# Kernel tuning notes

Measured on AMD Instinct MI355X. Metric: run time of the kernel, lower is better.

Reference implementation:

```python
import jax, jax.numpy as jnp
import numpy as np

N = 4096      # nodes
FEAT = 512    # feature_size
HID = 256     # hidden_dim
E = 131072    # edges (avg degree 32)


def setup_inputs() -> dict:
    key = jax.random.key(0)
    ks = jax.random.split(key, 10)
    x = jax.random.normal(ks[0], (N, FEAT), dtype=jnp.float32)
    edge_index = jax.random.randint(ks[1], (2, E), 0, N)
    edge_attr = jax.random.uniform(ks[2], (E, 1), dtype=jnp.float32)
    # nn.Linear(bias=False) weights, stored as [in, out] so k = x @ Wk
    Wk = jax.random.normal(ks[3], (FEAT, HID), dtype=jnp.float32) / np.sqrt(FEAT)
    Wq = jax.random.normal(ks[4], (FEAT, HID), dtype=jnp.float32) / np.sqrt(FEAT)
    Wv = jax.random.normal(ks[5], (FEAT, FEAT), dtype=jnp.float32) / np.sqrt(FEAT)
    # EmbeddingTable.reset_parameters: normal(0, 1), shape [num_embeddings=2, dim]
    Ek = jax.random.normal(ks[6], (2, HID), dtype=jnp.float32)
    Eq = jax.random.normal(ks[7], (2, HID), dtype=jnp.float32)
    Ev = jax.random.normal(ks[8], (2, FEAT), dtype=jnp.float32)
    # ContinuousEmbeddingIndex params
    idx_bias = jnp.full((1,), 0.5, dtype=jnp.float32)
    idx_mult = jnp.full((1,), 10.0, dtype=jnp.float32)
    return dict(x=x, edge_index=edge_index, edge_attr=edge_attr,
                Wk=Wk, Wq=Wq, Wv=Wv, Ek=Ek, Eq=Eq, Ev=Ev,
                idx_bias=idx_bias, idx_mult=idx_mult)


def reference(x, edge_index, edge_attr, Wk, Wq, Wv, Ek, Eq, Ev, idx_bias, idx_mult):
    n = x.shape[0]
    L = x.shape[-1]  # feature_size, used as softmax scale
    src, dst = edge_index[0], edge_index[1]

    # ContinuousEmbeddingIndex: soft 2-way interpolation weights [E, 2]
    s = jax.nn.sigmoid((edge_attr - idx_bias) * idx_mult)
    w = jnp.concatenate([s, 1.0 - s], axis=-1)

    # per-edge relative embeddings (EmbeddingTable: weights @ embeddings)
    rk = w @ Ek   # [E, HID]
    rq = w @ Eq   # [E, HID]
    rv = w @ Ev   # [E, FEAT]

    k = x @ Wk    # [N, HID]
    q = x @ Wq    # [N, HID]
    v = x @ Wv    # [N, FEAT]

    # A = q k^T + (q_i . Rk_ij) + (k_j . Rq_ij) + q k^T
    # The Rk/Rq terms are nonzero only on edges -> compute per-edge and scatter-add
    # (to_dense_adj sums duplicate edges, matched by .add).
    A = 2.0 * (q @ k.T)                                   # [N, N]
    edge_bias = jnp.sum(q[src] * rk, axis=-1) + jnp.sum(k[dst] * rq, axis=-1)  # [E]
    A = A.at[src, dst].add(edge_bias)
    A = jax.nn.softmax(A / np.sqrt(L), axis=-1)           # dropout = identity (eval)

    # M = A v + sum_j A_ij * Rv_ij  (second term only nonzero on edges)
    M = A @ v
    M = M + jax.ops.segment_sum(A[src, dst][:, None] * rv, src, num_segments=n)
    return M
```

## Files before the change

kernel.cpp:

```cpp
#include <hip/hip_runtime.h>
#include <hip/hip_bf16.h>
#include <cmath>


typedef short bf16x8 __attribute__((ext_vector_type(8)));
typedef float f32x4  __attribute__((ext_vector_type(4)));
typedef unsigned short ushort_t;
typedef unsigned short ushort8v __attribute__((ext_vector_type(8)));

constexpr int BUCKET = 64;

__device__ __forceinline__ ushort_t f2bf(float f) {
    union { float f; unsigned u; } v; v.f = f;
    unsigned u = v.u;
    u += 0x7FFFu + ((u >> 16) & 1u);
    return (ushort_t)(u >> 16);
}
__device__ __forceinline__ float bf2f(ushort_t h) {
    union { unsigned u; float f; } v; v.u = ((unsigned)h) << 16;
    return v.f;
}
__device__ __forceinline__ ushort_t f2h(float f) {
    union { _Float16 h; ushort_t u; } v; v.h = (_Float16)f; return v.u;
}
__device__ __forceinline__ float h2f(ushort_t u) {
    union { ushort_t u; _Float16 h; } v; v.u = u; return (float)v.h;
}
__device__ __forceinline__ void gload_lds16(const void* g, void* l) {
    __builtin_amdgcn_global_load_lds(
        (const __attribute__((address_space(1))) void*)g,
        (__attribute__((address_space(3))) void*)l, 16, 0, 0);
}

__device__ __forceinline__ void gemm_core(
    const ushort_t* __restrict__ A, const ushort_t* __restrict__ B,
    int lda, int ldb, int Ksz, size_t kbase, int bm, int bn,
    ushort_t* As, ushort_t* Bs, f32x4 (&acc)[4][4])
{
    constexpr int BK = 32;
    const int tid  = threadIdx.x;
    const int lane = tid & 63;
    const int wid  = tid >> 6;
    const int wm = (wid >> 1) * 64;
    const int wn = (wid & 1) * 64;

    const int r0 = tid >> 2;
    const int c8 = (tid & 3) * 8;
    const ushort_t* Ag0 = A + (size_t)(bm + r0) * lda + kbase + c8;
    const ushort_t* Bg0 = B + (size_t)(bn + r0) * ldb + kbase + c8;
    const ushort_t* Ag1 = Ag0 + (size_t)64 * lda;
    const ushort_t* Bg1 = Bg0 + (size_t)64 * ldb;
    ushort_t* AsW0 = &As[(wid * 64) * 8];
    ushort_t* AsW1 = &As[(256 + wid * 64) * 8];
    ushort_t* BsW0 = &Bs[(wid * 64) * 8];
    ushort_t* BsW1 = &Bs[(256 + wid * 64) * 8];

    const int fr = lane & 15;
    const int kh = (lane >> 4) * 8;

    for (int k0 = 0; k0 < Ksz; k0 += BK) {
        gload_lds16(Ag0 + k0, AsW0);
        gload_lds16(Ag1 + k0, AsW1);
        gload_lds16(Bg0 + k0, BsW0);
        gload_lds16(Bg1 + k0, BsW1);
        __syncthreads();

        bf16x8 af[4], bfv[4];
        #pragma unroll
        for (int i = 0; i < 4; ++i) {
            af[i]  = *(const bf16x8*)&As[(wm + i * 16 + fr) * 32 + kh];
            bfv[i] = *(const bf16x8*)&Bs[(wn + i * 16 + fr) * 32 + kh];
        }
        #pragma unroll
        for (int i = 0; i < 4; ++i)
            #pragma unroll
            for (int j = 0; j < 4; ++j)
                acc[i][j] = __builtin_amdgcn_mfma_f32_16x16x32_bf16(
                    af[i], bfv[j], acc[i][j], 0, 0, 0);
        __syncthreads();
    }
}

__device__ __forceinline__ int swizzle_bid()
{
    int bid = blockIdx.y * gridDim.x + blockIdx.x;
    const int nwg = gridDim.x * gridDim.y;
    if ((nwg & 7) == 0) {
        const int cpx = nwg >> 3;
        bid = (bid & 7) * cpx + (bid >> 3);
    }
    return bid;
}

template<int MODE>
__global__ __launch_bounds__(256) void gemm_nt_mfma(
    const ushort_t* __restrict__ A, const ushort_t* __restrict__ B,
    void* __restrict__ Cv, int lda, int ldb, int ldc, int Ksz, float alpha)
{
    __shared__ ushort_t As[128 * 32];
    __shared__ ushort_t Bs[128 * 32];
    const int bid = swizzle_bid();
    const int bm = (bid / gridDim.x) * 128;
    const int bn = (bid % gridDim.x) * 128;
    f32x4 acc[4][4] = {};
    gemm_core(A, B, lda, ldb, Ksz, 0, bm, bn, As, Bs, acc);

    const int lane = threadIdx.x & 63;
    const int wid  = threadIdx.x >> 6;
    const int wm = (wid >> 1) * 64, wn = (wid & 1) * 64;
    const int cr = (lane >> 4) * 4, cc = lane & 15;
    #pragma unroll
    for (int i = 0; i < 4; ++i)
        #pragma unroll
        for (int j = 0; j < 4; ++j) {
            const int col = bn + wn + j * 16 + cc;
            const int rowb = bm + wm + i * 16 + cr;
            #pragma unroll
            for (int jj = 0; jj < 4; ++jj) {
                const float val = alpha * acc[i][j][jj];
                if (MODE == 0)
                    ((float*)Cv)[(size_t)(rowb + jj) * ldc + col] = val;
                else if (MODE == 1)
                    ((ushort_t*)Cv)[(size_t)(rowb + jj) * ldc + col] = f2bf(val);
                else
                    ((ushort_t*)Cv)[(size_t)(rowb + jj) * ldc + col] = f2h(val);
            }
        }
}

__global__ __launch_bounds__(256) void proj_gemm(
    const ushort_t* __restrict__ xb, const ushort_t* __restrict__ Wqkt,
    const ushort_t* __restrict__ Wvt, ushort_t* __restrict__ qkb,
    ushort_t* __restrict__ vTb, int FEAT, int HID, int N)
{
    __shared__ ushort_t As[128 * 32];
    __shared__ ushort_t Bs[128 * 32];
    const int b = blockIdx.x;
    const ushort_t* A; const ushort_t* B; ushort_t* C;
    int bm, bn, ldc;
    if (b < 128) {
        const int gx = (2 * HID) / 128;
        bm = (b / gx) * 128; bn = (b % gx) * 128;
        A = xb; B = Wqkt; C = qkb; ldc = 2 * HID;
    } else {
        const int b2 = b - 128;
        const int gx = N / 128;
        bm = (b2 / gx) * 128; bn = (b2 % gx) * 128;
        A = Wvt; B = xb; C = vTb; ldc = N;
    }
    f32x4 acc[4][4] = {};
    gemm_core(A, B, FEAT, FEAT, FEAT, 0, bm, bn, As, Bs, acc);

    const int lane = threadIdx.x & 63;
    const int wid  = threadIdx.x >> 6;
    const int wm = (wid >> 1) * 64, wn = (wid & 1) * 64;
    const int cr = (lane >> 4) * 4, cc = lane & 15;
    #pragma unroll
    for (int i = 0; i < 4; ++i)
        #pragma unroll
        for (int j = 0; j < 4; ++j) {
            const int col = bn + wn + j * 16 + cc;
            const int rowb = bm + wm + i * 16 + cr;
            #pragma unroll
            for (int jj = 0; jj < 4; ++jj)
                C[(size_t)(rowb + jj) * ldc + col] = f2bf(acc[i][j][jj]);
        }
}

__global__ __launch_bounds__(256) void pv_gemm_splitk(
    const ushort_t* __restrict__ P, const ushort_t* __restrict__ vT,
    ushort_t* __restrict__ parts, int N, int FEAT, int Kchunk)
{
    __shared__ ushort_t As[128 * 32];
    __shared__ ushort_t Bs[128 * 32];
    const int bid = swizzle_bid();
    const int bm = (bid / gridDim.x) * 128;
    const int bn = (bid % gridDim.x) * 128;

    f32x4 acc[4][4] = {};
    gemm_core(P, vT, N, N, Kchunk, (size_t)blockIdx.z * Kchunk, bm, bn, As, Bs, acc);

    const int tid = threadIdx.x;
    const int lane = tid & 63;
    const int wid  = tid >> 6;
    const int wm = (wid >> 1) * 64, wn = (wid & 1) * 64;
    const int cr = (lane >> 4) * 4, cc = lane & 15;
    ushort_t* myPart = parts + (size_t)blockIdx.z * N * FEAT;
    #pragma unroll
    for (int i = 0; i < 4; ++i)
        #pragma unroll
        for (int j = 0; j < 4; ++j) {
            const int col = bn + wn + j * 16 + cc;
            const int rowb = bm + wm + i * 16 + cr;
            #pragma unroll
            for (int jj = 0; jj < 4; ++jj)
                myPart[(size_t)(rowb + jj) * FEAT + col] = f2bf(acc[i][j][jj]);
        }
}

__global__ void reduce_add_rv_kernel(
    const ushort_t* __restrict__ parts, float* __restrict__ out,
    const float* __restrict__ c0, const float* __restrict__ c1,
    const float* __restrict__ Ev, int FEAT, size_t zstride, int nz)
{
    const int i8 = blockIdx.x * 256 + threadIdx.x;
    const int F8 = FEAT / 8;
    const int node = i8 / F8;
    const int f0 = (i8 % F8) * 8;
    float s[8] = {};
    for (int z = 0; z < nz; ++z) {
        const ushort8v p = *(const ushort8v*)(parts + (size_t)z * zstride + (size_t)i8 * 8);
        #pragma unroll
        for (int j = 0; j < 8; ++j) s[j] += bf2f(p[j]);
    }
    const float a0 = c0[node], a1 = c1[node];
    float4 o0, o1;
    const float4 e00 = *(const float4*)(Ev + f0);
    const float4 e01 = *(const float4*)(Ev + f0 + 4);
    const float4 e10 = *(const float4*)(Ev + FEAT + f0);
    const float4 e11 = *(const float4*)(Ev + FEAT + f0 + 4);
    o0.x = s[0] + a0 * e00.x + a1 * e10.x;
    o0.y = s[1] + a0 * e00.y + a1 * e10.y;
    o0.z = s[2] + a0 * e00.z + a1 * e10.z;
    o0.w = s[3] + a0 * e00.w + a1 * e10.w;
    o1.x = s[4] + a0 * e01.x + a1 * e11.x;
    o1.y = s[5] + a0 * e01.y + a1 * e11.y;
    o1.z = s[6] + a0 * e01.z + a1 * e11.z;
    o1.w = s[7] + a0 * e01.w + a1 * e11.w;
    float* op = out + (size_t)node * FEAT + f0;
    *(float4*)op = o0;
    *(float4*)(op + 4) = o1;
}

__global__ __launch_bounds__(256) void prep_kernel(
    const float* __restrict__ x, const float* __restrict__ Wq,
    const float* __restrict__ Wk, const float* __restrict__ Wv,
    ushort_t* __restrict__ xb, ushort_t* __restrict__ Wqkt,
    ushort_t* __restrict__ Wvt, int* __restrict__ rowcnt,
    int N, int FEAT, int HID)
{
    const int b = blockIdx.x;
    const int tid = threadIdx.x;
    const int xBlocks = (N * FEAT / 8) / 256;
    const int qkTiles = (FEAT / 32) * (HID / 32);
    const int vTiles  = (FEAT / 32) * (FEAT / 32);
    const int zBase = xBlocks + 2 * qkTiles + vTiles;

    if (b >= zBase) {
        const int i = (b - zBase) * 256 + tid;
        if (i <= N) rowcnt[i] = 0;
        return;
    }
    if (b < xBlocks) {
        const int i = b * 256 + tid;
        const float4 a = ((const float4*)x)[2 * i];
        const float4 c = ((const float4*)x)[2 * i + 1];
        ushort8v o;
        o[0] = f2bf(a.x); o[1] = f2bf(a.y); o[2] = f2bf(a.z); o[3] = f2bf(a.w);
        o[4] = f2bf(c.x); o[5] = f2bf(c.y); o[6] = f2bf(c.z); o[7] = f2bf(c.w);
        ((ushort8v*)xb)[i] = o;
        return;
    }

    __shared__ float tile[32][33];
    int t = b - xBlocks;
    const float* src; ushort_t* dst; int I, O;
    if (t < qkTiles)            { src = Wq; dst = Wqkt;                       I = FEAT; O = HID; }
    else if (t < 2 * qkTiles)   { src = Wk; dst = Wqkt + (size_t)HID * FEAT;  I = FEAT; O = HID; t -= qkTiles; }
    else                        { src = Wv; dst = Wvt;                        I = FEAT; O = FEAT; t -= 2 * qkTiles; }
    const int ot = O / 32;
    const int r0 = (t / ot) * 32;
    const int c0 = (t % ot) * 32;
    const int lr = tid >> 5;
    const int lc = tid & 31;
    #pragma unroll
    for (int rr = 0; rr < 32; rr += 8)
        tile[lr + rr][lc] = src[(size_t)(r0 + lr + rr) * O + c0 + lc];
    __syncthreads();
    #pragma unroll
    for (int rr = 0; rr < 32; rr += 8)
        dst[(size_t)(c0 + lr + rr) * I + r0 + lc] = f2bf(tile[lc][lr + rr]);
}

__global__ __launch_bounds__(256) void node_dots(
    const ushort_t* __restrict__ qk,
    const float* __restrict__ Ek, const float* __restrict__ Eq,
    float* qk0, float* qk1, float* kq0, float* kq1, int HID)
{
    const int node = blockIdx.x;
    const int t = threadIdx.x;
    const ushort_t* row = qk + (size_t)node * (2 * HID);
    const float qv = bf2f(row[t]);
    const float kv = bf2f(row[HID + t]);
    float p0 = qv * Ek[t];
    float p1 = qv * Ek[HID + t];
    float p2 = kv * Eq[t];
    float p3 = kv * Eq[HID + t];
    #pragma unroll
    for (int off = 32; off > 0; off >>= 1) {
        p0 += __shfl_down(p0, off);
        p1 += __shfl_down(p1, off);
        p2 += __shfl_down(p2, off);
        p3 += __shfl_down(p3, off);
    }
    __shared__ float red[4][4];
    if ((t & 63) == 0) {
        const int w = t >> 6;
        red[w][0] = p0; red[w][1] = p1; red[w][2] = p2; red[w][3] = p3;
    }
    __syncthreads();
    if (t == 0) {
        qk0[node] = red[0][0] + red[1][0] + red[2][0] + red[3][0];
        qk1[node] = red[0][1] + red[1][1] + red[2][1] + red[3][1];
        kq0[node] = red[0][2] + red[1][2] + red[2][2] + red[3][2];
        kq1[node] = red[0][3] + red[1][3] + red[2][3] + red[3][3];
    }
}

__global__ void scatter_kernel(
    const int* __restrict__ ei, const float* __restrict__ attr,
    const float* __restrict__ qk0, const float* __restrict__ qk1,
    const float* __restrict__ kq0, const float* __restrict__ kq1,
    int* __restrict__ rowcnt, int4* __restrict__ ebuf, int4* __restrict__ oflow,
    int E, int N, float scale,
    const float* __restrict__ ibp, const float* __restrict__ imp)
{
    const int e = blockIdx.x * 256 + threadIdx.x;
    if (e >= E) return;
    const int src = ei[e];
    const int dst = ei[E + e];
    const float s = 1.f / (1.f + __expf(-(attr[e] - ibp[0]) * imp[0]));
    const float bias = (s * qk0[src] + (1.f - s) * qk1[src]
                      + s * kq0[dst] + (1.f - s) * kq1[dst]) * scale;
    const int pos = atomicAdd(&rowcnt[src], 1);
    if (pos < BUCKET) {
        int4 rec; rec.x = dst; rec.y = __float_as_int(bias);
        rec.z = __float_as_int(s); rec.w = 0;
        ebuf[(size_t)src * BUCKET + pos] = rec;
    } else {
        const int oi = atomicAdd(&rowcnt[N], 1);
        int4 rec; rec.x = src; rec.y = dst;
        rec.z = __float_as_int(bias); rec.w = __float_as_int(s);
        oflow[oi] = rec;
    }
}

__global__ __launch_bounds__(256) void softmax_rows_bf16(
    const ushort_t* __restrict__ Ah, const int* __restrict__ rowcnt,
    const int4* __restrict__ ebuf, const int4* __restrict__ oflow,
    ushort_t* __restrict__ P, float* __restrict__ c0, float* __restrict__ c1,
    int N)
{
    __shared__ float lbias[4096];
    __shared__ float red[4];
    __shared__ float csum[2];
    const int r = blockIdx.x;
    const ushort_t* a = Ah + (size_t)r * N;
    ushort_t* p = P + (size_t)r * N;
    const int t = threadIdx.x;

    #pragma unroll
    for (int u = 0; u < 4; ++u)
        *(float4*)&lbias[(u * 256 + t) * 4] = float4{0.f, 0.f, 0.f, 0.f};
    if (t < 2) csum[t] = 0.f;

    float v[16];
    {
        const ushort8v h0 = ((const ushort8v*)a)[t];
        const ushort8v h1 = ((const ushort8v*)a)[256 + t];
        #pragma unroll
        for (int j = 0; j < 8; ++j) { v[j] = h2f(h0[j]); v[8 + j] = h2f(h1[j]); }
    }
    __syncthreads();

    const int cnt = min(rowcnt[r], BUCKET);
    if (t < cnt) {
        const int4 rec = ebuf[(size_t)r * BUCKET + t];
        atomicAdd(&lbias[rec.x], __int_as_float(rec.y));
    }
    const int ocnt = rowcnt[N];
    for (int j = t; j < ocnt; j += 256) {
        const int4 rec = oflow[j];
        if (rec.x == r) atomicAdd(&lbias[rec.y], __int_as_float(rec.z));
    }
    __syncthreads();

    float mx = -1e30f;
    {
        const int b0 = t * 8, b1 = (256 + t) * 8;
        const float4 l0 = *(const float4*)&lbias[b0];
        const float4 l1 = *(const float4*)&lbias[b0 + 4];
        const float4 l2 = *(const float4*)&lbias[b1];
        const float4 l3 = *(const float4*)&lbias[b1 + 4];
        v[0] += l0.x; v[1] += l0.y; v[2]  += l0.z; v[3]  += l0.w;
        v[4] += l1.x; v[5] += l1.y; v[6]  += l1.z; v[7]  += l1.w;
        v[8] += l2.x; v[9] += l2.y; v[10] += l2.z; v[11] += l2.w;
        v[12] += l3.x; v[13] += l3.y; v[14] += l3.z; v[15] += l3.w;
    }
    #pragma unroll
    for (int j = 0; j < 16; ++j) mx = fmaxf(mx, v[j]);
    #pragma unroll
    for (int off = 32; off > 0; off >>= 1) mx = fmaxf(mx, __shfl_down(mx, off));
    if ((t & 63) == 0) red[t >> 6] = mx;
    __syncthreads();
    const float m = fmaxf(fmaxf(red[0], red[1]), fmaxf(red[2], red[3]));
    __syncthreads();

    float sum = 0.f;
    #pragma unroll
    for (int j = 0; j < 16; ++j) { v[j] = __expf(v[j] - m); sum += v[j]; }
    #pragma unroll
    for (int off = 32; off > 0; off >>= 1) sum += __shfl_down(sum, off);
    if ((t & 63) == 0) red[t >> 6] = sum;
    __syncthreads();
    const float inv = 1.f / (red[0] + red[1] + red[2] + red[3]);

    ushort8v o0, o1;
    {
        const int b0 = t * 8, b1 = (256 + t) * 8;
        #pragma unroll
        for (int j = 0; j < 8; ++j) {
            const float p0 = v[j] * inv;
            const float p1 = v[8 + j] * inv;
            o0[j] = f2bf(p0);
            o1[j] = f2bf(p1);
            lbias[b0 + j] = p0;
            lbias[b1 + j] = p1;
        }
    }
    ((ushort8v*)p)[t] = o0;
    ((ushort8v*)p)[256 + t] = o1;
    __syncthreads();

    if (t < cnt) {
        const int4 rec = ebuf[(size_t)r * BUCKET + t];
        const float s = __int_as_float(rec.z);
        const float pv = lbias[rec.x];
        atomicAdd(&csum[0], pv * s);
        atomicAdd(&csum[1], pv * (1.f - s));
    }
    for (int j = t; j < ocnt; j += 256) {
        const int4 rec = oflow[j];
        if (rec.x == r) {
            const float s = __int_as_float(rec.w);
            const float pv = lbias[rec.y];
            atomicAdd(&csum[0], pv * s);
            atomicAdd(&csum[1], pv * (1.f - s));
        }
    }
    __syncthreads();
    if (t == 0) { c0[r] = csum[0]; c1[r] = csum[1]; }
}

extern "C" void kernel_launch(void* const* d_in, const int* in_sizes, int n_in,
                              void* d_out, int out_size, void* d_ws, size_t ws_size,
                              hipStream_t stream)
{
    const float* x    = (const float*)d_in[0];
    const int*   ei   = (const int*)d_in[1];
    const float* attr = (const float*)d_in[2];
    const float* Wk   = (const float*)d_in[3];
    const float* Wq   = (const float*)d_in[4];
    const float* Wv   = (const float*)d_in[5];
    const float* Ek   = (const float*)d_in[6];
    const float* Eq   = (const float*)d_in[7];
    const float* Ev   = (const float*)d_in[8];
    const float* ib   = (const float*)d_in[9];
    const float* im   = (const float*)d_in[10];
    float* out = (float*)d_out;

    const int FEAT = (int)lroundf(sqrtf((float)in_sizes[5]));
    const int HID  = in_sizes[3] / FEAT;
    const int N    = in_sizes[0] / FEAT;
    const int E    = in_sizes[2];

    char* w = (char*)d_ws;
    size_t o = 0;
    ushort_t* xb   = (ushort_t*)(w + o); o += (size_t)N * FEAT * 2;
    ushort_t* Wqkt = (ushort_t*)(w + o); o += (size_t)2 * HID * FEAT * 2;
    ushort_t* Wvt  = (ushort_t*)(w + o); o += (size_t)FEAT * FEAT * 2;
    ushort_t* qkb  = (ushort_t*)(w + o); o += (size_t)N * 2 * HID * 2;
    ushort_t* vTb  = (ushort_t*)(w + o); o += (size_t)FEAT * N * 2;
    ushort_t* Ah   = (ushort_t*)(w + o); o += (size_t)N * N * 2;
    ushort_t* Pb   = (ushort_t*)(w + o); o += (size_t)N * N * 2;
    float*    qk0  = (float*)(w + o);    o += (size_t)N * 4;
    float*    qk1  = (float*)(w + o);    o += (size_t)N * 4;
    float*    kq0  = (float*)(w + o);    o += (size_t)N * 4;
    float*    kq1  = (float*)(w + o);    o += (size_t)N * 4;
    float*    c0   = (float*)(w + o);    o += (size_t)N * 4;
    float*    c1   = (float*)(w + o);    o += (size_t)N * 4;
    int*      rowcnt = (int*)(w + o);    o += (size_t)(N + 8) * 4;
    o = (o + 15) & ~(size_t)15;
    int4*     ebuf   = (int4*)(w + o);   o += (size_t)N * BUCKET * 16;
    int4*     oflow  = (int4*)(w + o);   o += (size_t)E * 16;
    ushort_t* pvpart = Ah;

    const dim3 blk(256);
    const int NZ = 4;
    const int Kchunk = N / NZ;
    const float scale = 1.f / sqrtf((float)FEAT);

    const int xBlocks = (N * FEAT / 8) / 256;
    const int qkTiles = (FEAT / 32) * (HID / 32);
    const int vTiles  = (FEAT / 32) * (FEAT / 32);
    const int zBlocks = (N + 1 + 255) / 256;
    prep_kernel<<<xBlocks + 2 * qkTiles + vTiles + zBlocks, blk, 0, stream>>>(
        x, Wq, Wk, Wv, xb, Wqkt, Wvt, rowcnt, N, FEAT, HID);

    proj_gemm<<<256, blk, 0, stream>>>(xb, Wqkt, Wvt, qkb, vTb, FEAT, HID, N);

    node_dots<<<N, blk, 0, stream>>>(qkb, Ek, Eq, qk0, qk1, kq0, kq1, HID);

    scatter_kernel<<<(E + 255) / 256, blk, 0, stream>>>(
        ei, attr, qk0, qk1, kq0, kq1, rowcnt, ebuf, oflow, E, N, scale, ib, im);

    gemm_nt_mfma<2><<<dim3(N / 128, N / 128), blk, 0, stream>>>(
        qkb, qkb + HID, Ah, 2 * HID, 2 * HID, N, HID, 2.f * scale);

    softmax_rows_bf16<<<N, blk, 0, stream>>>(Ah, rowcnt, ebuf, oflow, Pb, c0, c1, N);

    pv_gemm_splitk<<<dim3(FEAT / 128, N / 128, NZ), blk, 0, stream>>>(
        Pb, vTb, pvpart, N, FEAT, Kchunk);

    reduce_add_rv_kernel<<<(N * FEAT / 8) / 256, blk, 0, stream>>>(
        pvpart, out, c0, c1, Ev, FEAT, (size_t)N * FEAT, NZ);
}
```

Before: 118.5 us.

## Fuse node dot products into projection GEMM and merge scatter with QK GEMM

Computes the per-node Ek/Eq dot products in the projection GEMM epilogue, using 16-lane shuffle reductions followed by atomicAdd into zeroed buffers, and drops the separate node_dots kernel. The edge scatter and the QK^T GEMM are merged into one launch, with extra blocks beyond the GEMM tiles doing the scatter. This removes two kernel launches and lets the scatter's small blocks run alongside the GEMM tiles. The cost is float atomics in the epilogue (a non-deterministic summation order), extra zeroing work in the prep kernel, and the assumption that qk0/qk1/kq0/kq1 sit contiguously for dots4.

```diff
diff --git a/kernel.cpp b/kernel.cpp
--- a/kernel.cpp
+++ b/kernel.cpp
@@ -30,6 +30,13 @@
     __builtin_amdgcn_global_load_lds(
         (const __attribute__((address_space(1))) void*)g,
         (__attribute__((address_space(3))) void*)l, 16, 0, 0);
+}
+__device__ __forceinline__ float red16(float v) {
+    v += __shfl_down(v, 8, 16);
+    v += __shfl_down(v, 4, 16);
+    v += __shfl_down(v, 2, 16);
+    v += __shfl_down(v, 1, 16);
+    return v;
 }
 
 __device__ __forceinline__ void gemm_core(
@@ -81,10 +88,8 @@
     }
 }
 
-__device__ __forceinline__ int swizzle_bid()
-{
-    int bid = blockIdx.y * gridDim.x + blockIdx.x;
-    const int nwg = gridDim.x * gridDim.y;
+__device__ __forceinline__ int swizzle_n(int bid, int nwg)
+{
     if ((nwg & 7) == 0) {
         const int cpx = nwg >> 3;
         bid = (bid & 7) * cpx + (bid >> 3);
@@ -92,46 +97,14 @@
     return bid;
 }
 
-template<int MODE>
-__global__ __launch_bounds__(256) void gemm_nt_mfma(
-    const ushort_t* __restrict__ A, const ushort_t* __restrict__ B,
-    void* __restrict__ Cv, int lda, int ldb, int ldc, int Ksz, float alpha)
-{
-    __shared__ ushort_t As[128 * 32];
-    __shared__ ushort_t Bs[128 * 32];
-    const int bid = swizzle_bid();
-    const int bm = (bid / gridDim.x) * 128;
-    const int bn = (bid % gridDim.x) * 128;
-    f32x4 acc[4][4] = {};
-    gemm_core(A, B, lda, ldb, Ksz, 0, bm, bn, As, Bs, acc);
-
-    const int lane = threadIdx.x & 63;
-    const int wid  = threadIdx.x >> 6;
-    const int wm = (wid >> 1) * 64, wn = (wid & 1) * 64;
-    const int cr = (lane >> 4) * 4, cc = lane & 15;
-    #pragma unroll
-    for (int i = 0; i < 4; ++i)
-        #pragma unroll
-        for (int j = 0; j < 4; ++j) {
-            const int col = bn + wn + j * 16 + cc;
-            const int rowb = bm + wm + i * 16 + cr;
-            #pragma unroll
-            for (int jj = 0; jj < 4; ++jj) {
-                const float val = alpha * acc[i][j][jj];
-                if (MODE == 0)
-                    ((float*)Cv)[(size_t)(rowb + jj) * ldc + col] = val;
-                else if (MODE == 1)
-                    ((ushort_t*)Cv)[(size_t)(rowb + jj) * ldc + col] = f2bf(val);
-                else
-                    ((ushort_t*)Cv)[(size_t)(rowb + jj) * ldc + col] = f2h(val);
-            }
-        }
-}
-
 __global__ __launch_bounds__(256) void proj_gemm(
     const ushort_t* __restrict__ xb, const ushort_t* __restrict__ Wqkt,
     const ushort_t* __restrict__ Wvt, ushort_t* __restrict__ qkb,
-    ushort_t* __restrict__ vTb, int FEAT, int HID, int N)
+    ushort_t* __restrict__ vTb,
+    const float* __restrict__ Ek, const float* __restrict__ Eq,
+    float* __restrict__ qk0, float* __restrict__ qk1,
+    float* __restrict__ kq0, float* __restrict__ kq1,
+    int FEAT, int HID, int N)
 {
     __shared__ ushort_t As[128 * 32];
     __shared__ ushort_t Bs[128 * 32];
@@ -165,6 +138,96 @@
             for (int jj = 0; jj < 4; ++jj)
                 C[(size_t)(rowb + jj) * ldc + col] = f2bf(acc[i][j][jj]);
         }
+
+    if (b < 128) {
+        const bool isQ = (bn < 2 * HID / 2);
+        const float* W = isQ ? Ek : Eq;
+        float* d0 = isQ ? qk0 : kq0;
+        float* d1 = isQ ? qk1 : kq1;
+        const int hbase = bn - (isQ ? 0 : HID);
+        float w0[4], w1[4];
+        #pragma unroll
+        for (int j = 0; j < 4; ++j) {
+            const int h = hbase + wn + j * 16 + cc;
+            w0[j] = W[h];
+            w1[j] = W[HID + h];
+        }
+        #pragma unroll
+        for (int i = 0; i < 4; ++i)
+            #pragma unroll
+            for (int jj = 0; jj < 4; ++jj) {
+                float s0 = 0.f, s1 = 0.f;
+                #pragma unroll
+                for (int j = 0; j < 4; ++j) {
+                    const float v = acc[i][j][jj];
+                    s0 += v * w0[j];
+                    s1 += v * w1[j];
+                }
+                s0 = red16(s0);
+                s1 = red16(s1);
+                if ((lane & 15) == 0) {
+                    const int row = bm + wm + i * 16 + cr + jj;
+                    atomicAdd(&d0[row], s0);
+                    atomicAdd(&d1[row], s1);
+                }
+            }
+    }
+}
+
+__global__ __launch_bounds__(256) void sgemm_scatter(
+    const ushort_t* __restrict__ qkb, ushort_t* __restrict__ Ah,
+    const int* __restrict__ ei, const float* __restrict__ attr,
+    const float* __restrict__ qk0, const float* __restrict__ qk1,
+    const float* __restrict__ kq0, const float* __restrict__ kq1,
+    int* __restrict__ rowcnt, int4* __restrict__ ebuf, int4* __restrict__ oflow,
+    int N, int HID, int E, int gemmBlocks, float alpha, float scale,
+    const float* __restrict__ ibp, const float* __restrict__ imp)
+{
+    __shared__ ushort_t As[128 * 32];
+    __shared__ ushort_t Bs[128 * 32];
+    const int b = blockIdx.x;
+    if (b >= gemmBlocks) {
+        const int e = (b - gemmBlocks) * 256 + threadIdx.x;
+        if (e >= E) return;
+        const int src = ei[e];
+        const int dst = ei[E + e];
+        const float s = 1.f / (1.f + __expf(-(attr[e] - ibp[0]) * imp[0]));
+        const float bias = (s * qk0[src] + (1.f - s) * qk1[src]
+                          + s * kq0[dst] + (1.f - s) * kq1[dst]) * scale;
+        const int pos = atomicAdd(&rowcnt[src], 1);
+        if (pos < BUCKET) {
+            int4 rec; rec.x = dst; rec.y = __float_as_int(bias);
+            rec.z = __float_as_int(s); rec.w = 0;
+            ebuf[(size_t)src * BUCKET + pos] = rec;
+        } else {
+            const int oi = atomicAdd(&rowcnt[N], 1);
+            int4 rec; rec.x = src; rec.y = dst;
+            rec.z = __float_as_int(bias); rec.w = __float_as_int(s);
+            oflow[oi] = rec;
+        }
+        return;
+    }
+    const int gx = N / 128;
+    const int bid = swizzle_n(b, gemmBlocks);
+    const int bm = (bid / gx) * 128;
+    const int bn = (bid % gx) * 128;
+    f32x4 acc[4][4] = {};
+    gemm_core(qkb, qkb + HID, 2 * HID, 2 * HID, HID, 0, bm, bn, As, Bs, acc);
+
+    const int lane = threadIdx.x & 63;
+    const int wid  = threadIdx.x >> 6;
+    const int wm = (wid >> 1) * 64, wn = (wid & 1) * 64;
+    const int cr = (lane >> 4) * 4, cc = lane & 15;
+    #pragma unroll
+    for (int i = 0; i < 4; ++i)
+        #pragma unroll
+        for (int j = 0; j < 4; ++j) {
+            const int col = bn + wn + j * 16 + cc;
+            const int rowb = bm + wm + i * 16 + cr;
+            #pragma unroll
+            for (int jj = 0; jj < 4; ++jj)
+                Ah[(size_t)(rowb + jj) * N + col] = f2h(alpha * acc[i][j][jj]);
+        }
 }
 
 __global__ __launch_bounds__(256) void pv_gemm_splitk(
@@ -173,9 +236,10 @@
 {
     __shared__ ushort_t As[128 * 32];
     __shared__ ushort_t Bs[128 * 32];
-    const int bid = swizzle_bid();
-    const int bm = (bid / gridDim.x) * 128;
-    const int bn = (bid % gridDim.x) * 128;
+    const int gx = gridDim.x;
+    const int bid = swizzle_n(blockIdx.y * gx + blockIdx.x, gx * gridDim.y);
+    const int bm = (bid / gx) * 128;
+    const int bn = (bid % gx) * 128;
 
     f32x4 acc[4][4] = {};
     gemm_core(P, vT, N, N, Kchunk, (size_t)blockIdx.z * Kchunk, bm, bn, As, Bs, acc);
@@ -236,8 +300,8 @@
     const float* __restrict__ x, const float* __restrict__ Wq,
     const float* __restrict__ Wk, const float* __restrict__ Wv,
     ushort_t* __restrict__ xb, ushort_t* __restrict__ Wqkt,
-    ushort_t* __restrict__ Wvt, int* __restrict__ rowcnt,
-    int N, int FEAT, int HID)
+    ushort_t* __restrict__ Wvt, float* __restrict__ dots4,
+    int* __restrict__ rowcnt, int N, int FEAT, int HID)
 {
     const int b = blockIdx.x;
     const int tid = threadIdx.x;
@@ -248,7 +312,8 @@
 
     if (b >= zBase) {
         const int i = (b - zBase) * 256 + tid;
-        if (i <= N) rowcnt[i] = 0;
+        if (i < 4 * N) dots4[i] = 0.f;
+        else if (i <= 5 * N) rowcnt[i - 4 * N] = 0;
         return;
     }
     if (b < xBlocks) {
@@ -280,69 +345,6 @@
     #pragma unroll
     for (int rr = 0; rr < 32; rr += 8)
         dst[(size_t)(c0 + lr + rr) * I + r0 + lc] = f2bf(tile[lc][lr + rr]);
-}
-
-__global__ __launch_bounds__(256) void node_dots(
-    const ushort_t* __restrict__ qk,
-    const float* __restrict__ Ek, const float* __restrict__ Eq,
-    float* qk0, float* qk1, float* kq0, float* kq1, int HID)
-{
-    const int node = blockIdx.x;
-    const int t = threadIdx.x;
-    const ushort_t* row = qk + (size_t)node * (2 * HID);
-    const float qv = bf2f(row[t]);
-    const float kv = bf2f(row[HID + t]);
-    float p0 = qv * Ek[t];
-    float p1 = qv * Ek[HID + t];
-    float p2 = kv * Eq[t];
-    float p3 = kv * Eq[HID + t];
-    #pragma unroll
-    for (int off = 32; off > 0; off >>= 1) {
-        p0 += __shfl_down(p0, off);
-        p1 += __shfl_down(p1, off);
-        p2 += __shfl_down(p2, off);
-        p3 += __shfl_down(p3, off);
-    }
-    __shared__ float red[4][4];
-    if ((t & 63) == 0) {
-        const int w = t >> 6;
-        red[w][0] = p0; red[w][1] = p1; red[w][2] = p2; red[w][3] = p3;
-    }
-    __syncthreads();
-    if (t == 0) {
-        qk0[node] = red[0][0] + red[1][0] + red[2][0] + red[3][0];
-        qk1[node] = red[0][1] + red[1][1] + red[2][1] + red[3][1];
-        kq0[node] = red[0][2] + red[1][2] + red[2][2] + red[3][2];
-        kq1[node] = red[0][3] + red[1][3] + red[2][3] + red[3][3];
-    }
-}
-
-__global__ void scatter_kernel(
-    const int* __restrict__ ei, const float* __restrict__ attr,
-    const float* __restrict__ qk0, const float* __restrict__ qk1,
-    const float* __restrict__ kq0, const float* __restrict__ kq1,
-    int* __restrict__ rowcnt, int4* __restrict__ ebuf, int4* __restrict__ oflow,
-    int E, int N, float scale,
-    const float* __restrict__ ibp, const float* __restrict__ imp)
-{
-    const int e = blockIdx.x * 256 + threadIdx.x;
-    if (e >= E) return;
-    const int src = ei[e];
-    const int dst = ei[E + e];
-    const float s = 1.f / (1.f + __expf(-(attr[e] - ibp[0]) * imp[0]));
-    const float bias = (s * qk0[src] + (1.f - s) * qk1[src]
-                      + s * kq0[dst] + (1.f - s) * kq1[dst]) * scale;
-    const int pos = atomicAdd(&rowcnt[src], 1);
-    if (pos < BUCKET) {
-        int4 rec; rec.x = dst; rec.y = __float_as_int(bias);
-        rec.z = __float_as_int(s); rec.w = 0;
-        ebuf[(size_t)src * BUCKET + pos] = rec;
-    } else {
-        const int oi = atomicAdd(&rowcnt[N], 1);
-        int4 rec; rec.x = src; rec.y = dst;
-        rec.z = __float_as_int(bias); rec.w = __float_as_int(s);
-        oflow[oi] = rec;
-    }
 }
 
 __global__ __launch_bounds__(256) void softmax_rows_bf16(
@@ -503,19 +505,19 @@
     const int xBlocks = (N * FEAT / 8) / 256;
     const int qkTiles = (FEAT / 32) * (HID / 32);
     const int vTiles  = (FEAT / 32) * (FEAT / 32);
-    const int zBlocks = (N + 1 + 255) / 256;
+    const int zBlocks = (5 * N + 1 + 255) / 256;
     prep_kernel<<<xBlocks + 2 * qkTiles + vTiles + zBlocks, blk, 0, stream>>>(
-        x, Wq, Wk, Wv, xb, Wqkt, Wvt, rowcnt, N, FEAT, HID);
-
-    proj_gemm<<<256, blk, 0, stream>>>(xb, Wqkt, Wvt, qkb, vTb, FEAT, HID, N);
-
-    node_dots<<<N, blk, 0, stream>>>(qkb, Ek, Eq, qk0, qk1, kq0, kq1, HID);
-
-    scatter_kernel<<<(E + 255) / 256, blk, 0, stream>>>(
-        ei, attr, qk0, qk1, kq0, kq1, rowcnt, ebuf, oflow, E, N, scale, ib, im);
-
-    gemm_nt_mfma<2><<<dim3(N / 128, N / 128), blk, 0, stream>>>(
-        qkb, qkb + HID, Ah, 2 * HID, 2 * HID, N, HID, 2.f * scale);
+        x, Wq, Wk, Wv, xb, Wqkt, Wvt, qk0, rowcnt, N, FEAT, HID);
+
+    proj_gemm<<<256, blk, 0, stream>>>(xb, Wqkt, Wvt, qkb, vTb,
+                                       Ek, Eq, qk0, qk1, kq0, kq1,
+                                       FEAT, HID, N);
+
+    const int gemmBlocks = (N / 128) * (N / 128);
+    const int scatBlocks = (E + 255) / 256;
+    sgemm_scatter<<<gemmBlocks + scatBlocks, blk, 0, stream>>>(
+        qkb, Ah, ei, attr, qk0, qk1, kq0, kq1, rowcnt, ebuf, oflow,
+        N, HID, E, gemmBlocks, 2.f * scale, scale, ib, im);
 
     softmax_rows_bf16<<<N, blk, 0, stream>>>(Ah, rowcnt, ebuf, oflow, Pb, c0, c1, N);
 
```

New measurement: 111.0 us, median of 2. 6.3% less time.
